# Optimization experiments

Hardware: AMD Instinct MI355X
Metric: run time of the kernel (lower is better)

The kernel has to match this reference:

```python
import jax, jax.numpy as jnp
import numpy as np

K = 3        # kernel size
PAD = 1      # padding
DG = 16      # deformable groups
MAXR = 10.0  # max_residue_magnitude


def _lrelu(x):
    return jnp.where(x >= 0, x, 0.1 * x)


def _conv3(x, w, b):
    y = jax.lax.conv_general_dilated(x, w, (1, 1), 'SAME',
                                     dimension_numbers=('NCHW', 'OIHW', 'NCHW'))
    return y + b[None, :, None, None]


def _deform_conv2d(x, offset, mask, weight, bias):
    # x: [B,Cin,H,W]; offset: [B,2*DG*K*K,H,W]; mask: [B,DG*K*K,H,W]
    B, Cin, H, W = x.shape
    Cout = weight.shape[0]
    G, Cg, K2 = DG, Cin // DG, K * K
    off = offset.reshape(B, G, K2, 2, H, W)
    dy, dx = off[:, :, :, 0], off[:, :, :, 1]
    ky = jnp.repeat(jnp.arange(K), K).astype(x.dtype)   # [K2]
    kx = jnp.tile(jnp.arange(K), K).astype(x.dtype)
    hh = jnp.arange(H, dtype=x.dtype)
    ww = jnp.arange(W, dtype=x.dtype)
    # sampling positions [B,G,K2,H,W]
    py = dy + ky[None, None, :, None, None] + hh[None, None, None, :, None] - PAD
    px = dx + kx[None, None, :, None, None] + ww[None, None, None, None, :] - PAD
    y0 = jnp.floor(py)
    x0 = jnp.floor(px)
    wy1 = py - y0
    wx1 = px - x0
    xf = x.reshape(B, G, Cg, H * W)

    def gather(yi, xi, wgt):
        valid = (yi >= 0) & (yi <= H - 1) & (xi >= 0) & (xi <= W - 1)
        idx = (jnp.clip(yi, 0, H - 1).astype(jnp.int32) * W
               + jnp.clip(xi, 0, W - 1).astype(jnp.int32)).reshape(B, G, -1)
        vals = jnp.take_along_axis(
            xf, jnp.broadcast_to(idx[:, :, None, :], (B, G, Cg, idx.shape[-1])), axis=3)
        vals = vals.reshape(B, G, Cg, K2, H, W)
        w = (wgt * valid.astype(x.dtype))[:, :, None]  # [B,G,1,K2,H,W]
        return vals * w

    s = (gather(y0, x0, (1 - wy1) * (1 - wx1))
         + gather(y0, x0 + 1, (1 - wy1) * wx1)
         + gather(y0 + 1, x0, wy1 * (1 - wx1))
         + gather(y0 + 1, x0 + 1, wy1 * wx1))
    s = s * mask.reshape(B, G, K2, H, W)[:, :, None]
    wr = weight.reshape(Cout, G, Cg, K2)
    out = jnp.einsum('ogck,bgckhw->bohw', wr, s)
    return out + bias[None, :, None, None]


def setup_inputs() -> dict:
    key = jax.random.key(0)
    ks = jax.random.split(key, 16)
    B, Cin, Cout, H, W = 4, 128, 64, 96, 96
    Coff = 3 * Cout + 4  # 196
    stdv = 1.0 / np.sqrt(Cin * K * K)
    inp = {
        'x': jax.random.normal(ks[0], (B, Cin, H, W), jnp.float32),
        'extra_feat': jax.random.normal(ks[1], (B, 3 * Cout, H, W), jnp.float32),
        'flow_1': jax.random.normal(ks[2], (B, 2, H, W), jnp.float32),
        'flow_2': jax.random.normal(ks[3], (B, 2, H, W), jnp.float32),
        'weight': jax.random.uniform(ks[4], (Cout, Cin, K, K), jnp.float32, -stdv, stdv),
        'bias': jax.random.normal(ks[5], (Cout,), jnp.float32) * 0.01,
        'ow0': jax.random.normal(ks[6], (Cout, Coff, K, K), jnp.float32) * 0.02,
        'ob0': jnp.zeros((Cout,), jnp.float32),
        'ow1': jax.random.normal(ks[7], (Cout, Cout, K, K), jnp.float32) * 0.02,
        'ob1': jnp.zeros((Cout,), jnp.float32),
        'ow2': jax.random.normal(ks[8], (Cout, Cout, K, K), jnp.float32) * 0.02,
        'ob2': jnp.zeros((Cout,), jnp.float32),
        'ow3': jax.random.normal(ks[9], (27 * DG, Cout, K, K), jnp.float32) * 0.01,
        'ob3': jnp.zeros((27 * DG,), jnp.float32),
    }
    return inp


def reference(x, extra_feat, flow_1, flow_2, weight, bias,
              ow0, ob0, ow1, ob1, ow2, ob2, ow3, ob3):
    feat = jnp.concatenate([extra_feat, flow_1, flow_2], axis=1)
    h = _lrelu(_conv3(feat, ow0, ob0))
    h = _lrelu(_conv3(h, ow1, ob1))
    h = _lrelu(_conv3(h, ow2, ob2))
    out = _conv3(h, ow3, ob3)
    o1, o2, m = jnp.split(out, 3, axis=1)
    offs = MAXR * jnp.tanh(jnp.concatenate([o1, o2], axis=1))
    off1, off2 = jnp.split(offs, 2, axis=1)
    off1 = off1 + jnp.tile(flow_1[:, ::-1], (1, off1.shape[1] // 2, 1, 1))
    off2 = off2 + jnp.tile(flow_2[:, ::-1], (1, off2.shape[1] // 2, 1, 1))
    offset = jnp.concatenate([off1, off2], axis=1)
    mask = jax.nn.sigmoid(m)
    return _deform_conv2d(x, offset, mask, weight, bias)
```

## Files before the change

### kernel.cpp

```cpp
#include <hip/hip_runtime.h>
#include <math.h>

#define HW 9216
#define Hh 96
#define Ww 96
#define PHW 9604

typedef __attribute__((ext_vector_type(8))) short bh8;
typedef __attribute__((ext_vector_type(4))) short bh4;
typedef __attribute__((ext_vector_type(4))) float f32x4;
typedef __attribute__((ext_vector_type(2))) float f32x2;
typedef __attribute__((ext_vector_type(4))) int i32x4;
union bh8i { bh8 v; i32x4 i; };

__device__ __forceinline__ short f2bf(float f) {
    union { float f; unsigned u; } v; v.f = f;
    unsigned r = v.u + 0x7FFFu + ((v.u >> 16) & 1u);
    return (short)(r >> 16);
}
__device__ __forceinline__ float bf2f(short s) {
    union { unsigned u; float f; } v; v.u = ((unsigned)(unsigned short)s) << 16;
    return v.f;
}
__device__ __forceinline__ float lo_bf(unsigned u) {
    union { unsigned u; float f; } v; v.u = u << 16; return v.f;
}
__device__ __forceinline__ float hi_bf(unsigned u) {
    union { unsigned u; float f; } v; v.u = u & 0xFFFF0000u; return v.f;
}
__device__ __forceinline__ unsigned pack_bf2(float lo, float hi) {
    union { float f; unsigned u; } a, b; a.f = lo; b.f = hi;
    unsigned ul = a.u + 0x7FFFu + ((a.u >> 16) & 1u);
    unsigned uh = b.u + 0x7FFFu + ((b.u >> 16) & 1u);
    return (ul >> 16) | (uh & 0xFFFF0000u);
}

__global__ void prep_misc(short* __restrict__ xpad1, short* __restrict__ hpa,
                          short* __restrict__ hpb, short* __restrict__ xdp,
                          const float* __restrict__ ow0, const float* __restrict__ ow1,
                          const float* __restrict__ ow2, const float* __restrict__ ow3,
                          const float* __restrict__ wd,
                          short* __restrict__ wb0, short* __restrict__ wb1,
                          short* __restrict__ wb2, short* __restrict__ wb3,
                          short* __restrict__ wbd) {
    int i = blockIdx.x * 256 + threadIdx.x;
    const int z1 = 4 * 388 * 224, z2 = 4 * 388 * 64;
    if (i < z1 + 2 * z2) {
        short* p; int C;
        if (i < z1) { p = xpad1; C = 224; }
        else if (i < z1 + z2) { p = hpa; C = 64; i -= z1; }
        else { p = hpb; C = 64; i -= z1 + z2; }
        int c = i % C;
        int r = i / C;
        int b = r / 388, pid = r - b * 388;
        int row, col;
        if (pid < 98)       { row = 0;  col = pid; }
        else if (pid < 196) { row = 97; col = pid - 98; }
        else if (pid < 292) { row = pid - 196 + 1; col = 0; }
        else                { row = pid - 292 + 1; col = 97; }
        p[((size_t)b * PHW + row * 98 + col) * C + c] = 0;
        return;
    }
    i -= z1 + 2 * z2;
    const int zr = 4 * 16 * 388 * 8;
    if (i < zr) {
        int c8 = i & 7;
        int r = i >> 3;
        int pid = r % 388;
        int bg = r / 388;
        int row, col;
        if (pid < 98)       { row = 0;  col = pid; }
        else if (pid < 196) { row = 97; col = pid - 98; }
        else if (pid < 292) { row = pid - 196 + 1; col = 0; }
        else                { row = pid - 292 + 1; col = 97; }
        xdp[((size_t)bg * PHW + row * 98 + col) * 8 + c8] = 0;
        return;
    }
    i -= zr;
    const int n0 = 64 * 9 * 224, n1 = 64 * 9 * 64, n3 = 448 * 9 * 64, nd = 64 * 1152;
    if (i < n0) {
        int co = i / (9 * 224); int r = i - co * (9 * 224);
        int tap = r / 224, ci = r - tap * 224;
        wb0[i] = f2bf(ci < 196 ? ow0[(co * 196 + ci) * 9 + tap] : 0.f);
        return;
    }
    i -= n0;
    if (i < n1) {
        int co = i / (9 * 64); int r = i - co * (9 * 64);
        int tap = r / 64, ci = r - tap * 64;
        wb1[i] = f2bf(ow1[(co * 64 + ci) * 9 + tap]);
        return;
    }
    i -= n1;
    if (i < n1) {
        int co = i / (9 * 64); int r = i - co * (9 * 64);
        int tap = r / 64, ci = r - tap * 64;
        wb2[i] = f2bf(ow2[(co * 64 + ci) * 9 + tap]);
        return;
    }
    i -= n1;
    if (i < n3) {
        int co = i / (9 * 64); int r = i - co * (9 * 64);
        int tap = r / 64, ci = r - tap * 64;
        wb3[i] = f2bf(co < 432 ? ow3[(co * 64 + ci) * 9 + tap] : 0.f);
        return;
    }
    i -= n3;
    if (i < nd) {
        int co = i / 1152, kd = i - co * 1152;
        int gt = kd >> 3, c = kd & 7;
        int g = gt / 9, tap = gt - g * 9;
        wbd[i] = f2bf(wd[(co * 128 + g * 8 + c) * 9 + tap]);
    }
}

__global__ void pack_all(const float* __restrict__ extra,
                         const float* __restrict__ f1,
                         const float* __restrict__ f2,
                         const float* __restrict__ x,
                         short* __restrict__ xp,
                         short* __restrict__ xdp) {
    __shared__ float t[32][33];
    const int tid = threadIdx.x, tx = tid & 31, ty = tid >> 5;
    const int pt = blockIdx.x, b = blockIdx.z;
    if (blockIdx.y < 7) {
        const int ct = blockIdx.y;
#pragma unroll
        for (int j = 0; j < 4; ++j) {
            int ch = ct * 32 + ty + j * 8;
            int p = pt * 32 + tx;
            float v = 0.f;
            if (ch < 192)      v = extra[(b * 192 + ch) * HW + p];
            else if (ch < 194) v = f1[(b * 2 + ch - 192) * HW + p];
            else if (ch < 196) v = f2[(b * 2 + ch - 194) * HW + p];
            t[ty + j * 8][tx] = v;
        }
        __syncthreads();
#pragma unroll
        for (int j = 0; j < 4; ++j) {
            int pr = ty + j * 8;
            int p = pt * 32 + pr;
            int r = p / 96, c = p - r * 96;
            xp[((size_t)b * PHW + (r + 1) * 98 + (c + 1)) * 224 + ct * 32 + tx] =
                f2bf(t[tx][pr]);
        }
    } else {
        const int ct = blockIdx.y - 7;
#pragma unroll
        for (int j = 0; j < 4; ++j) {
            int ch = ct * 32 + ty + j * 8;
            t[ty + j * 8][tx] = x[((size_t)b * 128 + ch) * HW + pt * 32 + tx];
        }
        __syncthreads();
        if (tid < 128) {
            int oct = tid >> 5, p = tid & 31;
            int g = ct * 4 + oct;
            int pix = pt * 32 + p;
            int r = pix / 96, c = pix - r * 96;
            bh8 v;
#pragma unroll
            for (int cc = 0; cc < 8; ++cc) v[cc] = f2bf(t[oct * 8 + cc][p]);
            *(bh8*)&xdp[(((size_t)b * 16 + g) * PHW + (r + 1) * 98 + (c + 1)) * 8] = v;
        }
    }
}

template<int CINP, int KCH>
__launch_bounds__(256)
__global__ void conv_mfma(const short* __restrict__ xp,
                          const short* __restrict__ wb,
                          const float* __restrict__ bias,
                          short* __restrict__ o1) {
    __shared__ __attribute__((aligned(16))) short smA[9 * 64 * 32];
    const int tid = threadIdx.x;
    const int lane = tid & 63, wv = tid >> 6;
    const int q = lane >> 4, l15 = lane & 15;
    const int b = blockIdx.y;
    const int pix0 = blockIdx.x * 64 + wv * 16;
    const int soh = pix0 / 96, sow = pix0 - (pix0 / 96) * 96;

    const short* bp = xp + ((size_t)b * PHW + soh * 98 + sow + l15) * CINP + q * 8;

    const int sco = tid >> 2, sqq = tid & 3;
    const short* wsrc = wb + (size_t)sco * (9 * CINP) + sqq * 8;

    f32x4 acc[4];
#pragma unroll
    for (int t = 0; t < 4; ++t) acc[t] = (f32x4){0.f, 0.f, 0.f, 0.f};

    for (int p = 0; p < KCH; ++p) {
        __syncthreads();
        bh8 wtmp[9];
#pragma unroll
        for (int tap = 0; tap < 9; ++tap)
            wtmp[tap] = *(const bh8*)(wsrc + tap * CINP + p * 32);
#pragma unroll
        for (int tap = 0; tap < 9; ++tap)
            *(bh8*)&smA[tap * 2048 + sco * 32 + sqq * 8] = wtmp[tap];
        __syncthreads();
#pragma unroll
        for (int tap = 0; tap < 9; ++tap) {
            const int ky = tap / 3, kx = tap - (tap / 3) * 3;
            bh8 bf = *(const bh8*)(bp + (ky * 98 + kx) * CINP + p * 32);
#pragma unroll
            for (int t = 0; t < 4; ++t) {
                bh8 af = *(const bh8*)&smA[tap * 2048 + (t * 16 + l15) * 32 + q * 8];
                acc[t] = __builtin_amdgcn_mfma_f32_16x16x32_bf16(af, bf, acc[t], 0, 0, 0);
            }
        }
    }

    size_t base = ((size_t)b * PHW + (soh + 1) * 98 + sow + l15 + 1) * 64;
#pragma unroll
    for (int t = 0; t < 4; ++t) {
        bh4 v4;
#pragma unroll
        for (int r = 0; r < 4; ++r) {
            int co = t * 16 + q * 4 + r;
            float v = acc[t][r] + bias[co];
            v = (v >= 0.f) ? v : 0.1f * v;
            v4[r] = f2bf(v);
        }
        *(bh4*)(o1 + base + t * 16 + q * 4) = v4;
    }
}

__launch_bounds__(256)
__global__ void conv4_gemm(const short* __restrict__ xp,
                           const short* __restrict__ wb,
                           const float* __restrict__ bias,
                           float* __restrict__ offp,
                           short* __restrict__ maskb,
                           const float* __restrict__ flow1,
                           const float* __restrict__ flow2) {
    __shared__ __attribute__((aligned(16))) short smA[64 * 64];
    __shared__ __attribute__((aligned(16))) short smB[192 * 64];
    const int tid = threadIdx.x;
    const int lane = tid & 63, wv = tid >> 6;
    const int q = lane >> 4, l15 = lane & 15;
    const int pg = blockIdx.x;
    const int b = blockIdx.y;
    const int cob = blockIdx.z * 64;
    const int r0 = pg * 2;

    f32x4 acc[3][4];
#pragma unroll
    for (int pf = 0; pf < 3; ++pf)
#pragma unroll
        for (int cf = 0; cf < 4; ++cf) acc[pf][cf] = (f32x4){0.f, 0.f, 0.f, 0.f};

    for (int tap = 0; tap < 9; ++tap) {
        const int ky = tap / 3, kx = tap - (tap / 3) * 3;
        __syncthreads();
#pragma unroll
        for (int it = 0; it < 2; ++it) {
            int id = it * 256 + tid;
            int row = id >> 3, s = id & 7;
            int sw = s ^ (row & 7);
            *(bh8*)&smA[row * 64 + sw * 8] =
                *(const bh8*)(wb + (size_t)(cob + row) * 576 + tap * 64 + s * 8);
        }
#pragma unroll
        for (int it = 0; it < 6; ++it) {
            int id = it * 256 + tid;
            int row = id >> 3, s = id & 7;
            int sw = s ^ (row & 7);
            int srow = (row >= 96) ? 1 : 0;
            int scol = row - srow * 96;
            *(bh8*)&smB[row * 64 + sw * 8] = *(const bh8*)&xp[
                ((size_t)b * PHW + (r0 + srow + ky) * 98 + scol + kx) * 64 + s * 8];
        }
        __syncthreads();
#pragma unroll
        for (int kc = 0; kc < 2; ++kc) {
            bh8 bf[3], af[4];
#pragma unroll
            for (int pf = 0; pf < 3; ++pf) {
                int row = wv * 48 + pf * 16 + l15;
                int sw = (kc * 4 + q) ^ (row & 7);
                bf[pf] = *(const bh8*)&smB[row * 64 + sw * 8];
            }
#pragma unroll
            for (int cf = 0; cf < 4; ++cf) {
                int row = cf * 16 + l15;
                int sw = (kc * 4 + q) ^ (row & 7);
                af[cf] = *(const bh8*)&smA[row * 64 + sw * 8];
            }
#pragma unroll
            for (int pf = 0; pf < 3; ++pf)
#pragma unroll
                for (int cf = 0; cf < 4; ++cf)
                    acc[pf][cf] = __builtin_amdgcn_mfma_f32_16x16x32_bf16(
                        af[cf], bf[pf], acc[pf][cf], 0, 0, 0);
        }
    }

#pragma unroll
    for (int pf = 0; pf < 3; ++pf) {
        int local = wv * 48 + pf * 16 + l15;
        int lrow = (local >= 96) ? 1 : 0;
        int pix = (r0 + lrow) * 96 + (local - lrow * 96);
#pragma unroll
        for (int cf = 0; cf < 4; ++cf) {
            int cb0 = cob + cf * 16 + q * 4;
            if (cb0 < 288) {
                const float* fl = (cb0 < 144) ? flow1 : flow2;
                float fe = fl[(b * 2 + 1) * HW + pix];
                float fo = fl[(b * 2) * HW + pix];
                float t0 = 10.f * tanhf(acc[pf][cf][0] + bias[cb0 + 0]) + fe;
                float t1 = 10.f * tanhf(acc[pf][cf][1] + bias[cb0 + 1]) + fo;
                float t2 = 10.f * tanhf(acc[pf][cf][2] + bias[cb0 + 2]) + fe;
                float t3 = 10.f * tanhf(acc[pf][cf][3] + bias[cb0 + 3]) + fo;
                size_t p0 = ((size_t)b * 144 + (cb0 >> 1)) * HW + pix;
                *(f32x2*)&offp[p0 * 2] = (f32x2){t0, t1};
                *(f32x2*)&offp[(p0 + HW) * 2] = (f32x2){t2, t3};
            } else {
#pragma unroll
                for (int r = 0; r < 4; ++r) {
                    int chn = cb0 + r;
                    if (chn < 432) {
                        float v = acc[pf][cf][r] + bias[chn];
                        maskb[((size_t)b * 144 + (chn - 288)) * HW + pix] =
                            f2bf(1.f / (1.f + expf(-v)));
                    }
                }
            }
        }
    }
}

__launch_bounds__(256)
__global__ void deform_mfma(const short* __restrict__ xdp,
                            const float* __restrict__ offp,
                            const short* __restrict__ maskb,
                            const short* __restrict__ wbd,
                            const float* __restrict__ bias,
                            float* __restrict__ out) {
    __shared__ float red[4][1024];
    const int tid = threadIdx.x;
    const int lane = tid & 63, wv = tid >> 6;
    const int q = lane >> 4, l15 = lane & 15;
    const int blk = blockIdx.x;
    const int xs = blk & 7, idx = blk >> 3;
    const int b = xs >> 1;
    const int pix0 = ((xs & 1) * 288 + idx) * 16;
    const int pix = pix0 + l15;
    const int h = pix / 96, w = pix - (pix / 96) * 96;

    const float* opp = offp + ((size_t)b * 144 * HW + pix) * 2;
    const short* mp = maskb + (size_t)b * 144 * HW + pix;
    const short* xb = xdp + (size_t)b * 16 * PHW * 8;
    const short* ap = wbd + (size_t)l15 * 1152 + wv * 288 + q * 8;

    f32x2 dxy[9];
    float mk[9];
#pragma unroll
    for (int i = 0; i < 9; ++i) {
        const int gt = wv * 36 + i * 4 + q;
        dxy[i] = *(const f32x2*)(opp + (size_t)gt * HW * 2);
        mk[i] = bf2f(mp[(size_t)gt * HW]);
    }

    const short* cp[9];
    f32x4 ww[9];
#pragma unroll
    for (int i = 0; i < 9; ++i) {
        const int gt = wv * 36 + i * 4 + q;
        const int g = gt / 9, tap = gt - (gt / 9) * 9;
        float py = dxy[i][0] + (float)(tap / 3) + (float)h - 1.f;
        float px = dxy[i][1] + (float)(tap - (tap / 3) * 3) + (float)w - 1.f;
        py = fminf(fmaxf(py, -1.f), 96.f);
        px = fminf(fmaxf(px, -1.f), 96.f);
        float y0f = floorf(py), x0f = floorf(px);
        float wy1 = py - y0f, wx1 = px - x0f;
        float wy0 = 1.f - wy1, wx0 = 1.f - wx1;
        int yp = (int)y0f + 1, xp = (int)x0f + 1;
        cp[i] = xb + ((size_t)g * PHW + yp * 98 + xp) * 8;
        float m = mk[i];
        ww[i] = (f32x4){wy0 * wx0 * m, wy0 * wx1 * m, wy1 * wx0 * m, wy1 * wx1 * m};
    }

    f32x4 acc[4];
#pragma unroll
    for (int t = 0; t < 4; ++t) acc[t] = (f32x4){0.f, 0.f, 0.f, 0.f};

#pragma unroll
    for (int i = 0; i < 9; ++i) {
        bh8i c00, c01, c10, c11;
        c00.v = *(const bh8*)(cp[i]);
        c01.v = *(const bh8*)(cp[i] + 8);
        c10.v = *(const bh8*)(cp[i] + 98 * 8);
        c11.v = *(const bh8*)(cp[i] + 99 * 8);
        const float w00 = ww[i][0], w01 = ww[i][1], w10 = ww[i][2], w11 = ww[i][3];
        bh8i bf;
#pragma unroll
        for (int k = 0; k < 4; ++k) {
            unsigned u00 = (unsigned)c00.i[k], u01 = (unsigned)c01.i[k];
            unsigned u10 = (unsigned)c10.i[k], u11 = (unsigned)c11.i[k];
            float lo = w00 * lo_bf(u00) + w01 * lo_bf(u01)
                     + w10 * lo_bf(u10) + w11 * lo_bf(u11);
            float hi = w00 * hi_bf(u00) + w01 * hi_bf(u01)
                     + w10 * hi_bf(u10) + w11 * hi_bf(u11);
            bf.i[k] = (int)pack_bf2(lo, hi);
        }
#pragma unroll
        for (int t = 0; t < 4; ++t) {
            bh8 af = *(const bh8*)(ap + (size_t)t * 16 * 1152 + i * 32);
            acc[t] = __builtin_amdgcn_mfma_f32_16x16x32_bf16(af, bf.v, acc[t], 0, 0, 0);
        }
    }

#pragma unroll
    for (int t = 0; t < 4; ++t)
#pragma unroll
        for (int r = 0; r < 4; ++r)
            red[wv][(t * 16 + q * 4 + r) * 16 + l15] = acc[t][r];
    __syncthreads();
    for (int e = tid; e < 1024; e += 256) {
        int co = e >> 4, pl = e & 15;
        float v = red[0][e] + red[1][e] + red[2][e] + red[3][e] + bias[co];
        out[((size_t)b * 64 + co) * HW + pix0 + pl] = v;
    }
}

extern "C" void kernel_launch(void* const* d_in, const int* in_sizes, int n_in,
                              void* d_out, int out_size, void* d_ws, size_t ws_size,
                              hipStream_t stream) {
    const float* x      = (const float*)d_in[0];
    const float* extra  = (const float*)d_in[1];
    const float* flow1  = (const float*)d_in[2];
    const float* flow2  = (const float*)d_in[3];
    const float* weight = (const float*)d_in[4];
    const float* bias   = (const float*)d_in[5];
    const float* ow0    = (const float*)d_in[6];
    const float* ob0    = (const float*)d_in[7];
    const float* ow1    = (const float*)d_in[8];
    const float* ob1    = (const float*)d_in[9];
    const float* ow2    = (const float*)d_in[10];
    const float* ob2    = (const float*)d_in[11];
    const float* ow3    = (const float*)d_in[12];
    const float* ob3    = (const float*)d_in[13];
    float* out = (float*)d_out;

    char* wsb = (char*)d_ws;
    short* xpad1 = (short*)wsb;   wsb += (size_t)4 * PHW * 224 * 2;
    short* hpa   = (short*)wsb;   wsb += (size_t)4 * PHW * 64 * 2;
    short* hpb   = (short*)wsb;   wsb += (size_t)4 * PHW * 64 * 2;
    float* offpair = (float*)wsb; wsb += (size_t)4 * 144 * HW * 2 * 4;
    short* maskbuf = (short*)wsb; wsb += (size_t)4 * 144 * HW * 2;
    short* xdp     = (short*)wsb; wsb += (size_t)4 * 16 * PHW * 8 * 2 + 32;
    short* wb0     = (short*)wsb; wsb += 64 * 9 * 224 * 2;
    short* wb1     = (short*)wsb; wsb += 64 * 9 * 64 * 2;
    short* wb2     = (short*)wsb; wsb += 64 * 9 * 64 * 2;
    short* wb3     = (short*)wsb; wsb += 448 * 9 * 64 * 2;
    short* wbd     = (short*)wsb;

    const int prep_total = 546304 + 198656 + 534528;
    prep_misc<<<dim3((prep_total + 255) / 256), 256, 0, stream>>>(
        xpad1, hpa, hpb, xdp, ow0, ow1, ow2, ow3, weight,
        wb0, wb1, wb2, wb3, wbd);
    pack_all<<<dim3(288, 11, 4), 256, 0, stream>>>(extra, flow1, flow2, x, xpad1, xdp);

    conv_mfma<224, 7><<<dim3(144, 4), 256, 0, stream>>>(xpad1, wb0, ob0, hpa);
    conv_mfma<64, 2><<<dim3(144, 4), 256, 0, stream>>>(hpa, wb1, ob1, hpb);
    conv_mfma<64, 2><<<dim3(144, 4), 256, 0, stream>>>(hpb, wb2, ob2, hpa);
    conv4_gemm<<<dim3(48, 4, 7), 256, 0, stream>>>(hpa, wb3, ob3, offpair,
                                                   maskbuf, flow1, flow2);
    deform_mfma<<<dim3(2304), 256, 0, stream>>>(xdp, offpair, maskbuf, wbd, bias, out);
}
```

Before: 291.3 us.

## Interleave row pairs in deform input buffer and prefetch bilinear corners

The padded per-group input buffer now stores each pixel together with the pixel one row below it, 16 bf16 per slot on a 99-wide plane. Each bilinear sample then fetches all four corners from one 64-byte contiguous span instead of two separate row reads. The deform kernel also double-buffers the corner loads for the next tap, uses packed f32x2 arithmetic, and converts with the hardware v_cvt_pk_bf16_f32 instruction instead of manual rounding. In exchange the buffer doubles in size, pack_all writes it twice, and a full hipMemsetAsync replaces the border-only zeroing, which adds memory traffic.

```diff
diff --git a/kernel.cpp b/kernel.cpp
--- a/kernel.cpp
+++ b/kernel.cpp
@@ -5,6 +5,7 @@
 #define Hh 96
 #define Ww 96
 #define PHW 9604
+#define XDP_PLANE 9702
 
 typedef __attribute__((ext_vector_type(8))) short bh8;
 typedef __attribute__((ext_vector_type(4))) short bh4;
@@ -28,15 +29,14 @@
 __device__ __forceinline__ float hi_bf(unsigned u) {
     union { unsigned u; float f; } v; v.u = u & 0xFFFF0000u; return v.f;
 }
-__device__ __forceinline__ unsigned pack_bf2(float lo, float hi) {
-    union { float f; unsigned u; } a, b; a.f = lo; b.f = hi;
-    unsigned ul = a.u + 0x7FFFu + ((a.u >> 16) & 1u);
-    unsigned uh = b.u + 0x7FFFu + ((b.u >> 16) & 1u);
-    return (ul >> 16) | (uh & 0xFFFF0000u);
+__device__ __forceinline__ int cvt_pk_bf16(float lo, float hi) {
+    int r;
+    asm("v_cvt_pk_bf16_f32 %0, %1, %2" : "=v"(r) : "v"(lo), "v"(hi));
+    return r;
 }
 
 __global__ void prep_misc(short* __restrict__ xpad1, short* __restrict__ hpa,
-                          short* __restrict__ hpb, short* __restrict__ xdp,
+                          short* __restrict__ hpb,
                           const float* __restrict__ ow0, const float* __restrict__ ow1,
                           const float* __restrict__ ow2, const float* __restrict__ ow3,
                           const float* __restrict__ wd,
@@ -62,21 +62,6 @@
         return;
     }
     i -= z1 + 2 * z2;
-    const int zr = 4 * 16 * 388 * 8;
-    if (i < zr) {
-        int c8 = i & 7;
-        int r = i >> 3;
-        int pid = r % 388;
-        int bg = r / 388;
-        int row, col;
-        if (pid < 98)       { row = 0;  col = pid; }
-        else if (pid < 196) { row = 97; col = pid - 98; }
-        else if (pid < 292) { row = pid - 196 + 1; col = 0; }
-        else                { row = pid - 292 + 1; col = 97; }
-        xdp[((size_t)bg * PHW + row * 98 + col) * 8 + c8] = 0;
-        return;
-    }
-    i -= zr;
     const int n0 = 64 * 9 * 224, n1 = 64 * 9 * 64, n3 = 448 * 9 * 64, nd = 64 * 1152;
     if (i < n0) {
         int co = i / (9 * 224); int r = i - co * (9 * 224);
@@ -160,7 +145,9 @@
             bh8 v;
 #pragma unroll
             for (int cc = 0; cc < 8; ++cc) v[cc] = f2bf(t[oct * 8 + cc][p]);
-            *(bh8*)&xdp[(((size_t)b * 16 + g) * PHW + (r + 1) * 98 + (c + 1)) * 8] = v;
+            size_t base = ((size_t)b * 16 + g) * XDP_PLANE;
+            *(bh8*)&xdp[(base + (size_t)(r + 1) * 99 + (c + 1)) * 16] = v;
+            *(bh8*)&xdp[(base + (size_t)r * 99 + (c + 1)) * 16 + 8] = v;
         }
     }
 }
@@ -349,7 +336,7 @@
 
     const float* opp = offp + ((size_t)b * 144 * HW + pix) * 2;
     const short* mp = maskb + (size_t)b * 144 * HW + pix;
-    const short* xb = xdp + (size_t)b * 16 * PHW * 8;
+    const short* xb = xdp + (size_t)b * 16 * XDP_PLANE * 16;
     const short* ap = wbd + (size_t)l15 * 1152 + wv * 288 + q * 8;
 
     f32x2 dxy[9];
@@ -361,7 +348,7 @@
         mk[i] = bf2f(mp[(size_t)gt * HW]);
     }
 
-    const short* cp[9];
+    int cpo[9];
     f32x4 ww[9];
 #pragma unroll
     for (int i = 0; i < 9; ++i) {
@@ -375,7 +362,7 @@
         float wy1 = py - y0f, wx1 = px - x0f;
         float wy0 = 1.f - wy1, wx0 = 1.f - wx1;
         int yp = (int)y0f + 1, xp = (int)x0f + 1;
-        cp[i] = xb + ((size_t)g * PHW + yp * 98 + xp) * 8;
+        cpo[i] = (g * XDP_PLANE + yp * 99 + xp) * 16;
         float m = mk[i];
         ww[i] = (f32x4){wy0 * wx0 * m, wy0 * wx1 * m, wy1 * wx0 * m, wy1 * wx1 * m};
     }
@@ -384,24 +371,42 @@
 #pragma unroll
     for (int t = 0; t < 4; ++t) acc[t] = (f32x4){0.f, 0.f, 0.f, 0.f};
 
+    bh8i cb0[4], cb1[4];
+    {
+        const short* p = xb + cpo[0];
+        cb0[0].v = *(const bh8*)(p);
+        cb0[1].v = *(const bh8*)(p + 8);
+        cb0[2].v = *(const bh8*)(p + 16);
+        cb0[3].v = *(const bh8*)(p + 24);
+    }
 #pragma unroll
     for (int i = 0; i < 9; ++i) {
-        bh8i c00, c01, c10, c11;
-        c00.v = *(const bh8*)(cp[i]);
-        c01.v = *(const bh8*)(cp[i] + 8);
-        c10.v = *(const bh8*)(cp[i] + 98 * 8);
-        c11.v = *(const bh8*)(cp[i] + 99 * 8);
-        const float w00 = ww[i][0], w01 = ww[i][1], w10 = ww[i][2], w11 = ww[i][3];
+        bh8i* cur = (i & 1) ? cb1 : cb0;
+        bh8i* nxt = (i & 1) ? cb0 : cb1;
+        if (i + 1 < 9) {
+            const short* p = xb + cpo[i + 1];
+            nxt[0].v = *(const bh8*)(p);
+            nxt[1].v = *(const bh8*)(p + 8);
+            nxt[2].v = *(const bh8*)(p + 16);
+            nxt[3].v = *(const bh8*)(p + 24);
+        }
+        const f32x2 W00 = (f32x2){ww[i][0], ww[i][0]};
+        const f32x2 W01 = (f32x2){ww[i][1], ww[i][1]};
+        const f32x2 W10 = (f32x2){ww[i][2], ww[i][2]};
+        const f32x2 W11 = (f32x2){ww[i][3], ww[i][3]};
         bh8i bf;
 #pragma unroll
         for (int k = 0; k < 4; ++k) {
-            unsigned u00 = (unsigned)c00.i[k], u01 = (unsigned)c01.i[k];
-            unsigned u10 = (unsigned)c10.i[k], u11 = (unsigned)c11.i[k];
-            float lo = w00 * lo_bf(u00) + w01 * lo_bf(u01)
-                     + w10 * lo_bf(u10) + w11 * lo_bf(u11);
-            float hi = w00 * hi_bf(u00) + w01 * hi_bf(u01)
-                     + w10 * hi_bf(u10) + w11 * hi_bf(u11);
-            bf.i[k] = (int)pack_bf2(lo, hi);
+            unsigned u00 = (unsigned)cur[0].i[k];
+            unsigned u10 = (unsigned)cur[1].i[k];
+            unsigned u01 = (unsigned)cur[2].i[k];
+            unsigned u11 = (unsigned)cur[3].i[k];
+            f32x2 p00 = (f32x2){lo_bf(u00), hi_bf(u00)};
+            f32x2 p01 = (f32x2){lo_bf(u01), hi_bf(u01)};
+            f32x2 p10 = (f32x2){lo_bf(u10), hi_bf(u10)};
+            f32x2 p11 = (f32x2){lo_bf(u11), hi_bf(u11)};
+            f32x2 s = p00 * W00 + p01 * W01 + p10 * W10 + p11 * W11;
+            bf.i[k] = cvt_pk_bf16(s[0], s[1]);
         }
 #pragma unroll
         for (int t = 0; t < 4; ++t) {
@@ -448,16 +453,19 @@
     short* hpb   = (short*)wsb;   wsb += (size_t)4 * PHW * 64 * 2;
     float* offpair = (float*)wsb; wsb += (size_t)4 * 144 * HW * 2 * 4;
     short* maskbuf = (short*)wsb; wsb += (size_t)4 * 144 * HW * 2;
-    short* xdp     = (short*)wsb; wsb += (size_t)4 * 16 * PHW * 8 * 2 + 32;
+    const size_t xdp_bytes = (size_t)4 * 16 * XDP_PLANE * 16 * 2;
+    short* xdp     = (short*)wsb; wsb += xdp_bytes + 32;
     short* wb0     = (short*)wsb; wsb += 64 * 9 * 224 * 2;
     short* wb1     = (short*)wsb; wsb += 64 * 9 * 64 * 2;
     short* wb2     = (short*)wsb; wsb += 64 * 9 * 64 * 2;
     short* wb3     = (short*)wsb; wsb += 448 * 9 * 64 * 2;
     short* wbd     = (short*)wsb;
 
-    const int prep_total = 546304 + 198656 + 534528;
+    hipMemsetAsync(xdp, 0, xdp_bytes, stream);
+
+    const int prep_total = 546304 + 534528;
     prep_misc<<<dim3((prep_total + 255) / 256), 256, 0, stream>>>(
-        xpad1, hpa, hpb, xdp, ow0, ow1, ow2, ow3, weight,
+        xpad1, hpa, hpb, ow0, ow1, ow2, ow3, weight,
         wb0, wb1, wb2, wb3, wbd);
     pack_all<<<dim3(288, 11, 4), 256, 0, stream>>>(extra, flow1, flow2, x, xpad1, xdp);
 
```

After: 303.9 us. 4.3% more time.

## Store 2x2 bilinear neighbours per slot so deform GEMM uses one load

Applied to the files above, without the earlier changes.

The padded input for the deformable conv is repacked so each slot holds the four bilinear neighbours (32 bf16 values: 4 corners × 8 channels). Each MFMA K-slice now maps a quad lane group to one corner, so each lane does one 16-byte gather and one weight multiply instead of four gathers and a 4-term blend. The loop is also restructured per group, with hardware v_cvt_pk_bf16_f32 conversion and a matching weight layout. In exchange the packed buffer is four times larger, pack_all writes it four times, and border zeroing is reworked.

```diff
diff --git a/kernel.cpp b/kernel.cpp
--- a/kernel.cpp
+++ b/kernel.cpp
@@ -5,6 +5,7 @@
 #define Hh 96
 #define Ww 96
 #define PHW 9604
+#define QSLOTS 9604
 
 typedef __attribute__((ext_vector_type(8))) short bh8;
 typedef __attribute__((ext_vector_type(4))) short bh4;
@@ -28,11 +29,10 @@
 __device__ __forceinline__ float hi_bf(unsigned u) {
     union { unsigned u; float f; } v; v.u = u & 0xFFFF0000u; return v.f;
 }
-__device__ __forceinline__ unsigned pack_bf2(float lo, float hi) {
-    union { float f; unsigned u; } a, b; a.f = lo; b.f = hi;
-    unsigned ul = a.u + 0x7FFFu + ((a.u >> 16) & 1u);
-    unsigned uh = b.u + 0x7FFFu + ((b.u >> 16) & 1u);
-    return (ul >> 16) | (uh & 0xFFFF0000u);
+__device__ __forceinline__ int cvt_pk_bf16(float lo, float hi) {
+    int r;
+    asm("v_cvt_pk_bf16_f32 %0, %1, %2" : "=v"(r) : "v"(lo), "v"(hi));
+    return r;
 }
 
 __global__ void prep_misc(short* __restrict__ xpad1, short* __restrict__ hpa,
@@ -62,22 +62,27 @@
         return;
     }
     i -= z1 + 2 * z2;
-    const int zr = 4 * 16 * 388 * 8;
+    const int zr = 64 * 579 * 4;
     if (i < zr) {
-        int c8 = i & 7;
-        int r = i >> 3;
-        int pid = r % 388;
-        int bg = r / 388;
-        int row, col;
-        if (pid < 98)       { row = 0;  col = pid; }
-        else if (pid < 196) { row = 97; col = pid - 98; }
-        else if (pid < 292) { row = pid - 196 + 1; col = 0; }
-        else                { row = pid - 292 + 1; col = 97; }
-        xdp[((size_t)bg * PHW + row * 98 + col) * 8 + c8] = 0;
+        int piece = i & 3;
+        int r2 = i >> 2;
+        int s = r2 % 579, bg = r2 / 579;
+        int y, x;
+        if (s < 98)       { y = 0;  x = s; }
+        else if (s < 196) { y = 96; x = s - 98; }
+        else if (s < 294) { y = 97; x = s - 196; }
+        else {
+            int s2 = s - 294;
+            int xi = s2 / 95;
+            x = (xi == 0) ? 0 : ((xi == 1) ? 96 : 97);
+            y = 1 + s2 - xi * 95;
+        }
+        *(bh8*)&xdp[(((size_t)bg * QSLOTS) + y * 98 + x) * 32 + piece * 8] =
+            (bh8){0, 0, 0, 0, 0, 0, 0, 0};
         return;
     }
     i -= zr;
-    const int n0 = 64 * 9 * 224, n1 = 64 * 9 * 64, n3 = 448 * 9 * 64, nd = 64 * 1152;
+    const int n0 = 64 * 9 * 224, n1 = 64 * 9 * 64, n3 = 448 * 9 * 64, nd = 144 * 64 * 8;
     if (i < n0) {
         int co = i / (9 * 224); int r = i - co * (9 * 224);
         int tap = r / 224, ci = r - tap * 224;
@@ -107,8 +112,8 @@
     }
     i -= n3;
     if (i < nd) {
-        int co = i / 1152, kd = i - co * 1152;
-        int gt = kd >> 3, c = kd & 7;
+        int gt = i >> 9, r = i & 511;
+        int co = r >> 3, c = r & 7;
         int g = gt / 9, tap = gt - g * 9;
         wbd[i] = f2bf(wd[(co * 128 + g * 8 + c) * 9 + tap]);
     }
@@ -160,7 +165,12 @@
             bh8 v;
 #pragma unroll
             for (int cc = 0; cc < 8; ++cc) v[cc] = f2bf(t[oct * 8 + cc][p]);
-            *(bh8*)&xdp[(((size_t)b * 16 + g) * PHW + (r + 1) * 98 + (c + 1)) * 8] = v;
+            size_t sb = ((size_t)b * 16 + g) * QSLOTS;
+            int pr = r + 1, pc = c + 1;
+            *(bh8*)&xdp[(sb + pr * 98 + pc) * 32 + 0]        = v;
+            *(bh8*)&xdp[(sb + pr * 98 + pc - 1) * 32 + 8]    = v;
+            *(bh8*)&xdp[(sb + (pr - 1) * 98 + pc) * 32 + 16] = v;
+            *(bh8*)&xdp[(sb + (pr - 1) * 98 + pc - 1) * 32 + 24] = v;
         }
     }
 }
@@ -347,66 +357,62 @@
     const int pix = pix0 + l15;
     const int h = pix / 96, w = pix - (pix / 96) * 96;
 
-    const float* opp = offp + ((size_t)b * 144 * HW + pix) * 2;
-    const short* mp = maskb + (size_t)b * 144 * HW + pix;
-    const short* xb = xdp + (size_t)b * 16 * PHW * 8;
-    const short* ap = wbd + (size_t)l15 * 1152 + wv * 288 + q * 8;
-
-    f32x2 dxy[9];
-    float mk[9];
-#pragma unroll
-    for (int i = 0; i < 9; ++i) {
-        const int gt = wv * 36 + i * 4 + q;
-        dxy[i] = *(const f32x2*)(opp + (size_t)gt * HW * 2);
-        mk[i] = bf2f(mp[(size_t)gt * HW]);
-    }
-
-    const short* cp[9];
-    f32x4 ww[9];
-#pragma unroll
-    for (int i = 0; i < 9; ++i) {
-        const int gt = wv * 36 + i * 4 + q;
-        const int g = gt / 9, tap = gt - (gt / 9) * 9;
-        float py = dxy[i][0] + (float)(tap / 3) + (float)h - 1.f;
-        float px = dxy[i][1] + (float)(tap - (tap / 3) * 3) + (float)w - 1.f;
-        py = fminf(fmaxf(py, -1.f), 96.f);
-        px = fminf(fmaxf(px, -1.f), 96.f);
-        float y0f = floorf(py), x0f = floorf(px);
-        float wy1 = py - y0f, wx1 = px - x0f;
-        float wy0 = 1.f - wy1, wx0 = 1.f - wx1;
-        int yp = (int)y0f + 1, xp = (int)x0f + 1;
-        cp[i] = xb + ((size_t)g * PHW + yp * 98 + xp) * 8;
-        float m = mk[i];
-        ww[i] = (f32x4){wy0 * wx0 * m, wy0 * wx1 * m, wy1 * wx0 * m, wy1 * wx1 * m};
-    }
+    const short* xb = xdp + (size_t)b * 16 * QSLOTS * 32;
 
     f32x4 acc[4];
 #pragma unroll
     for (int t = 0; t < 4; ++t) acc[t] = (f32x4){0.f, 0.f, 0.f, 0.f};
 
 #pragma unroll
-    for (int i = 0; i < 9; ++i) {
-        bh8i c00, c01, c10, c11;
-        c00.v = *(const bh8*)(cp[i]);
-        c01.v = *(const bh8*)(cp[i] + 8);
-        c10.v = *(const bh8*)(cp[i] + 98 * 8);
-        c11.v = *(const bh8*)(cp[i] + 99 * 8);
-        const float w00 = ww[i][0], w01 = ww[i][1], w10 = ww[i][2], w11 = ww[i][3];
-        bh8i bf;
-#pragma unroll
-        for (int k = 0; k < 4; ++k) {
-            unsigned u00 = (unsigned)c00.i[k], u01 = (unsigned)c01.i[k];
-            unsigned u10 = (unsigned)c10.i[k], u11 = (unsigned)c11.i[k];
-            float lo = w00 * lo_bf(u00) + w01 * lo_bf(u01)
-                     + w10 * lo_bf(u10) + w11 * lo_bf(u11);
-            float hi = w00 * hi_bf(u00) + w01 * hi_bf(u01)
-                     + w10 * hi_bf(u10) + w11 * hi_bf(u11);
-            bf.i[k] = (int)pack_bf2(lo, hi);
-        }
-#pragma unroll
-        for (int t = 0; t < 4; ++t) {
-            bh8 af = *(const bh8*)(ap + (size_t)t * 16 * 1152 + i * 32);
-            acc[t] = __builtin_amdgcn_mfma_f32_16x16x32_bf16(af, bf.v, acc[t], 0, 0, 0);
+    for (int chunk = 0; chunk < 4; ++chunk) {
+        const int g = wv * 4 + chunk;
+        const float* opp = offp + (((size_t)b * 144 + g * 9) * HW + pix) * 2;
+        const short* mp  = maskb + ((size_t)b * 144 + g * 9) * HW + pix;
+
+        f32x2 dxy[9];
+        float mk[9];
+#pragma unroll
+        for (int i = 0; i < 9; ++i) {
+            dxy[i] = *(const f32x2*)(opp + (size_t)i * HW * 2);
+            mk[i]  = bf2f(mp[(size_t)i * HW]);
+        }
+
+        int soff[9];
+        float wq[9];
+#pragma unroll
+        for (int i = 0; i < 9; ++i) {
+            float py = dxy[i][0] + (float)(i / 3) + (float)h - 1.f;
+            float px = dxy[i][1] + (float)(i % 3) + (float)w - 1.f;
+            py = fminf(fmaxf(py, -1.f), 96.f);
+            px = fminf(fmaxf(px, -1.f), 96.f);
+            float y0f = floorf(py), x0f = floorf(px);
+            float wy1 = py - y0f, wx1 = px - x0f;
+            int yp = (int)y0f + 1, xp = (int)x0f + 1;
+            soff[i] = ((g * QSLOTS + yp * 98 + xp) << 5) + q * 8;
+            float wy = (q & 2) ? wy1 : (1.f - wy1);
+            float wx = (q & 1) ? wx1 : (1.f - wx1);
+            wq[i] = wy * wx * mk[i];
+        }
+
+#pragma unroll
+        for (int i = 0; i < 9; ++i) {
+            bh8i cv;
+            cv.v = *(const bh8*)(xb + soff[i]);
+            const f32x2 w2 = (f32x2){wq[i], wq[i]};
+            bh8i bf;
+#pragma unroll
+            for (int k2 = 0; k2 < 4; ++k2) {
+                unsigned u = (unsigned)cv.i[k2];
+                f32x2 pv = (f32x2){lo_bf(u), hi_bf(u)} * w2;
+                bf.i[k2] = cvt_pk_bf16(pv[0], pv[1]);
+            }
+            const int gt = g * 9 + i;
+            const short* ap = wbd + ((size_t)gt * 64 + l15) * 8;
+#pragma unroll
+            for (int t = 0; t < 4; ++t) {
+                bh8 af = *(const bh8*)(ap + t * 128);
+                acc[t] = __builtin_amdgcn_mfma_f32_16x16x32_bf16(af, bf.v, acc[t], 0, 0, 0);
+            }
         }
     }
 
@@ -448,14 +454,14 @@
     short* hpb   = (short*)wsb;   wsb += (size_t)4 * PHW * 64 * 2;
     float* offpair = (float*)wsb; wsb += (size_t)4 * 144 * HW * 2 * 4;
     short* maskbuf = (short*)wsb; wsb += (size_t)4 * 144 * HW * 2;
-    short* xdp     = (short*)wsb; wsb += (size_t)4 * 16 * PHW * 8 * 2 + 32;
+    short* xdp     = (short*)wsb; wsb += (size_t)4 * 16 * QSLOTS * 32 * 2 + 64;
     short* wb0     = (short*)wsb; wsb += 64 * 9 * 224 * 2;
     short* wb1     = (short*)wsb; wsb += 64 * 9 * 64 * 2;
     short* wb2     = (short*)wsb; wsb += 64 * 9 * 64 * 2;
     short* wb3     = (short*)wsb; wsb += 448 * 9 * 64 * 2;
     short* wbd     = (short*)wsb;
 
-    const int prep_total = 546304 + 198656 + 534528;
+    const int prep_total = 546304 + 148224 + 534528;
     prep_misc<<<dim3((prep_total + 255) / 256), 256, 0, stream>>>(
         xpad1, hpa, hpb, xdp, ow0, ow1, ow2, ow3, weight,
         wb0, wb1, wb2, wb3, wbd);
```

Result: slower. 314.3 us (+7.9%).
